# Kernel tuning notes

Measured on AMD Instinct MI355X. Metric: run time of the kernel, lower is better.

## Reference

```python
import jax, jax.numpy as jnp
import numpy as np

B, T, N, D = 1, 128, 32768, 1024


def setup_inputs() -> dict:
    key = jax.random.key(0)
    k1, k2 = jax.random.split(key)
    inputs = jax.random.normal(k1, (B, N, D), dtype=jnp.float32)
    # Nested tag->token coverage: tag i covers tokens [i*s, N). This guarantees
    # each tag keeps s exclusive tokens after the 'direct string' deduction,
    # so the row-normalization never divides by zero (matches real DOM data).
    s = N // T
    tok = jnp.arange(N)
    ttt = (tok[None, :] >= (jnp.arange(T) * s)[:, None]).astype(jnp.float32)  # (T, N)
    tag_to_token = jnp.broadcast_to(ttt[None], (B, T, N)).astype(jnp.float32)
    # Tag adjacency: self-loops + sparse random children.
    rand = jax.random.bernoulli(k2, 0.05, (T, T))
    gat_mask = (jnp.eye(T, dtype=bool) | rand).astype(jnp.int32)[None]  # (B, T, T)
    return {"inputs": inputs, "tag_to_token": tag_to_token, "gat_mask": gat_mask}


def deduce_direct_string(tag_to_token):
    # temp[i] = binary[i] - sum_{j>i} binary[j]  (original loop reads unmodified suffix rows)
    binary = (tag_to_token > 0).astype(tag_to_token.dtype)
    suffix_incl = jnp.flip(jnp.cumsum(jnp.flip(binary, axis=1), axis=1), axis=1)
    temp = binary - (suffix_incl - binary)
    temp = jnp.where(temp > 0, temp, 0.0)
    return temp / jnp.sum(temp, axis=2, keepdims=True)


def deduce_child(gat_mask):
    # Faithful to the torch nested loop (valid for B == 1).
    L = gat_mask.shape[1]

    def outer(i, child):
        child = child.at[:, i].set(gat_mask[:, i])

        def inner(j, c):
            temp = c[:, j][:, None, :] * gat_mask[:, j][:, None, :]  # (B,1,L)
            return ((c - temp) > 0).astype(c.dtype)

        return jax.lax.fori_loop(i + 1, L, inner, child)

    return jax.lax.fori_loop(0, L, outer, jnp.zeros_like(gat_mask))


def reference(inputs, tag_to_token, gat_mask):
    gm = gat_mask.astype(inputs.dtype)
    t2t = deduce_direct_string(tag_to_token)          # (B, T, N)
    child = deduce_child(gm)                          # (B, T, T)
    outputs = jnp.matmul(t2t, inputs)                 # (B, T, D)
    Tn = outputs.shape[1]

    # Triangular recurrence, i = T-1 ... 0; row i reads already-updated rows > i.
    def step(o, i):
        row = jnp.einsum('bt,btd->bd', child[:, i], o)
        return o.at[:, i].set(row), None

    outputs, _ = jax.lax.scan(step, outputs, jnp.arange(Tn - 1, -1, -1))
    return outputs
```

## Files before the change

### kernel.cpp

```cpp
#include <hip/hip_runtime.h>

#define NTOK 32768
#define NTAG 128
#define DDIM 1024
#define TPB 32


__global__ __launch_bounds__(256) void k_zero(const int* __restrict__ gm,
                                              float* __restrict__ P,
                                              int* __restrict__ cnt,
                                              unsigned* __restrict__ maskT) {
    const int tid = threadIdx.x;
    const int gid = blockIdx.x * 256 + tid;
    reinterpret_cast<float4*>(P)[gid] = make_float4(0.f, 0.f, 0.f, 0.f);
    if (gid < NTAG) cnt[gid] = 0;

    if (blockIdx.x == 1 || blockIdx.x == 2) {
        const int idx = (blockIdx.x - 1) * 256 + tid;
        const int l = idx & 15;
        const int iw = (idx >> 4) & 3;
        const int k = idx >> 6;
        const int colg = 16 * k + l;
        unsigned w = 0;
#pragma unroll
        for (int ib = 0; ib < 32; ++ib)
            w |= (unsigned)(gm[(iw * 32 + ib) * NTAG + colg] != 0) << ib;
        maskT[idx] = w;
    }
}

__global__ __launch_bounds__(256) void k_fused(const float* __restrict__ inp,
                                               const float* __restrict__ t2t,
                                               float* __restrict__ P,
                                               int* __restrict__ cnt) {
    __shared__ int part[8][TPB];
    __shared__ int tags[TPB];
    const int tid = threadIdx.x;
    const int n0 = blockIdx.x * TPB;

    {
        const int c = tid >> 5;
        const int n = tid & 31;
        int m = -1;
#pragma unroll
        for (int j = 0; j < 16; ++j) {
            const int r = c * 16 + j;
            if (t2t[(size_t)r * NTOK + n0 + n] > 0.f) m = r;
        }
        part[c][n] = m;
    }
    __syncthreads();
    if (tid < TPB) {
        int m = -1;
#pragma unroll
        for (int cc = 0; cc < 8; ++cc) m = max(m, part[cc][tid]);
        tags[tid] = m;
    }
    __syncthreads();

    const int col = tid * 4;
    const float4* src = reinterpret_cast<const float4*>(inp) + (size_t)n0 * 256 + tid;

    float4 acc = make_float4(0.f, 0.f, 0.f, 0.f);
    int cur = tags[0];
    int runlen = 0;

#pragma unroll
    for (int half = 0; half < 2; ++half) {
        float4 v[16];
#pragma unroll
        for (int k = 0; k < 16; ++k)
            v[k] = src[(size_t)(half * 16 + k) * 256];
#pragma unroll
        for (int k = 0; k < 16; ++k) {
            const int tg = tags[half * 16 + k];
            if (tg != cur) {
                if (cur >= 0) {
                    float* p = P + (size_t)cur * DDIM + col;
                    atomicAdd(p + 0, acc.x);
                    atomicAdd(p + 1, acc.y);
                    atomicAdd(p + 2, acc.z);
                    atomicAdd(p + 3, acc.w);
                    if (tid == 0) atomicAdd(&cnt[cur], runlen);
                }
                acc = make_float4(0.f, 0.f, 0.f, 0.f);
                cur = tg;
                runlen = 0;
            }
            if (tg >= 0) {
                acc.x += v[k].x;
                acc.y += v[k].y;
                acc.z += v[k].z;
                acc.w += v[k].w;
                ++runlen;
            }
        }
    }
    if (cur >= 0) {
        float* p = P + (size_t)cur * DDIM + col;
        atomicAdd(p + 0, acc.x);
        atomicAdd(p + 1, acc.y);
        atomicAdd(p + 2, acc.z);
        atomicAdd(p + 3, acc.w);
        if (tid == 0) atomicAdd(&cnt[cur], runlen);
    }
}

template <int CTRL>
__device__ __forceinline__ float dpp_add(float x) {
    const int y = __builtin_amdgcn_update_dpp(0, __float_as_int(x), CTRL, 0xF, 0xF, true);
    return x + __int_as_float(y);
}

__global__ __launch_bounds__(64, 1) void k_recur(const float* __restrict__ P,
                                                 const unsigned* __restrict__ maskT,
                                                 const int* __restrict__ cnt,
                                                 float* __restrict__ out) {
    __shared__ float xpose[NTAG][5];
    const int L = threadIdx.x;
    const int g = L >> 4;
    const int l = L & 15;
    const int c0 = blockIdx.x * 4;

    unsigned mw[8][4];
#pragma unroll
    for (int k = 0; k < 8; ++k)
#pragma unroll
        for (int iw = 0; iw < 4; ++iw) mw[k][iw] = maskT[(k * 4 + iw) * 16 + l];

    const float ia = 1.0f / (float)cnt[L];
    const float ib_ = 1.0f / (float)cnt[64 + L];
    float4 pa = *reinterpret_cast<const float4*>(P + (size_t)L * DDIM + c0);
    float4 pb = *reinterpret_cast<const float4*>(P + (size_t)(64 + L) * DDIM + c0);
    xpose[L][0] = pa.x * ia;
    xpose[L][1] = pa.y * ia;
    xpose[L][2] = pa.z * ia;
    xpose[L][3] = pa.w * ia;
    xpose[64 + L][0] = pb.x * ib_;
    xpose[64 + L][1] = pb.y * ib_;
    xpose[64 + L][2] = pb.z * ib_;
    xpose[64 + L][3] = pb.w * ib_;
    __syncthreads();

    float o0 = xpose[l][g], o1 = xpose[16 + l][g];
    float o2 = xpose[32 + l][g], o3 = xpose[48 + l][g];
    float o4 = xpose[64 + l][g], o5 = xpose[80 + l][g];
    float o6 = xpose[96 + l][g], o7 = xpose[112 + l][g];

#define SECTION(IW, KU, IBHI, IBLO)                                         \
    _Pragma("unroll 2") for (int ib = IBHI; ib >= IBLO; --ib) {             \
        float sa = (float)((mw[0][IW] >> ib) & 1u) * o0;                    \
        sa += (float)((mw[1][IW] >> ib) & 1u) * o1;                         \
        sa += (float)((mw[2][IW] >> ib) & 1u) * o2;                         \
        sa += (float)((mw[3][IW] >> ib) & 1u) * o3;                         \
        float sb = (float)((mw[4][IW] >> ib) & 1u) * o4;                    \
        sb += (float)((mw[5][IW] >> ib) & 1u) * o5;                         \
        sb += (float)((mw[6][IW] >> ib) & 1u) * o6;                         \
        sb += (float)((mw[7][IW] >> ib) & 1u) * o7;                         \
        float s = sa + sb;                                                  \
        s = dpp_add<0xB1>(s);                           \
        s = dpp_add<0x4E>(s);                           \
        s = dpp_add<0x141>(s);                         \
        s = dpp_add<0x140>(s);  \
        if (l == (ib & 15)) o##KU = s;                                      \
    }

    SECTION(3, 7, 31, 16)
    SECTION(3, 6, 15, 0)
    SECTION(2, 5, 31, 16)
    SECTION(2, 4, 15, 0)
    SECTION(1, 3, 31, 16)
    SECTION(1, 2, 15, 0)
    SECTION(0, 1, 31, 16)
    SECTION(0, 0, 15, 0)
#undef SECTION

    __syncthreads();
    xpose[l][g] = o0;
    xpose[16 + l][g] = o1;
    xpose[32 + l][g] = o2;
    xpose[48 + l][g] = o3;
    xpose[64 + l][g] = o4;
    xpose[80 + l][g] = o5;
    xpose[96 + l][g] = o6;
    xpose[112 + l][g] = o7;
    __syncthreads();
    float4 ra, rb;
    ra.x = xpose[L][0];
    ra.y = xpose[L][1];
    ra.z = xpose[L][2];
    ra.w = xpose[L][3];
    rb.x = xpose[64 + L][0];
    rb.y = xpose[64 + L][1];
    rb.z = xpose[64 + L][2];
    rb.w = xpose[64 + L][3];
    *reinterpret_cast<float4*>(out + (size_t)L * DDIM + c0) = ra;
    *reinterpret_cast<float4*>(out + (size_t)(64 + L) * DDIM + c0) = rb;
}

extern "C" void kernel_launch(void* const* d_in, const int* in_sizes, int n_in,
                              void* d_out, int out_size, void* d_ws, size_t ws_size,
                              hipStream_t stream) {
    const float* inp = (const float*)d_in[0];
    const float* t2t = (const float*)d_in[1];
    const int* gm = (const int*)d_in[2];
    float* out = (float*)d_out;

    char* ws = (char*)d_ws;
    float* P = (float*)ws;
    int* cnt = (int*)(ws + 524288);
    unsigned* maskT = (unsigned*)(ws + 524800);

    k_zero<<<128, 256, 0, stream>>>(gm, P, cnt, maskT);
    k_fused<<<NTOK / TPB, 256, 0, stream>>>(inp, t2t, P, cnt);
    k_recur<<<DDIM / 4, 64, 0, stream>>>(P, maskT, cnt, out);
}
```

Measured before the change: 51.22 us.

## Precompute blocked triangular resolvent to batch recurrence in groups of eight rows

A setup kernel now solves each 8x8 diagonal block of the mask recurrence ahead of time and stores float coefficient rows RT, one row per tag. With those coefficients, the recurrence kernel can compute eight rows together from the group's pre-update values instead of running 128 strictly serial dependent steps. This shortens the critical dependency chain and lets the eight DPP reductions per group overlap. In exchange, each group reads float4 coefficient rows from global memory instead of bitmasks held in registers, and the zeroing launch shrinks from 128 blocks to 16.

```diff
diff --git a/kernel.cpp b/kernel.cpp
--- a/kernel.cpp
+++ b/kernel.cpp
@@ -6,27 +6,41 @@
 #define TPB 32
 
 
-__global__ __launch_bounds__(256) void k_zero(const int* __restrict__ gm,
-                                              float* __restrict__ P,
-                                              int* __restrict__ cnt,
-                                              unsigned* __restrict__ maskT) {
-    const int tid = threadIdx.x;
-    const int gid = blockIdx.x * 256 + tid;
-    reinterpret_cast<float4*>(P)[gid] = make_float4(0.f, 0.f, 0.f, 0.f);
-    if (gid < NTAG) cnt[gid] = 0;
-
-    if (blockIdx.x == 1 || blockIdx.x == 2) {
-        const int idx = (blockIdx.x - 1) * 256 + tid;
-        const int l = idx & 15;
-        const int iw = (idx >> 4) & 3;
-        const int k = idx >> 6;
-        const int colg = 16 * k + l;
-        unsigned w = 0;
-#pragma unroll
-        for (int ib = 0; ib < 32; ++ib)
-            w |= (unsigned)(gm[(iw * 32 + ib) * NTAG + colg] != 0) << ib;
-        maskT[idx] = w;
-    }
+__global__ __launch_bounds__(128) void k_rt(const int* __restrict__ gm,
+                                            float* __restrict__ P,
+                                            int* __restrict__ cnt,
+                                            float* __restrict__ RT) {
+    __shared__ float rt[8][NTAG];
+    __shared__ float gblk[8][8];
+    const int t = threadIdx.x;
+    const int b = blockIdx.x;
+    const int g0 = b * 8;
+
+    float4* P4 = reinterpret_cast<float4*>(P) + b * 2048 + t;
+#pragma unroll
+    for (int q = 0; q < 16; ++q) P4[q * 128] = make_float4(0.f, 0.f, 0.f, 0.f);
+    if (b == 0) cnt[t] = 0;
+
+    if (t < 64) gblk[t >> 3][t & 7] =
+        (float)(gm[(g0 + (t >> 3)) * NTAG + g0 + (t & 7)] != 0);
+    float grows[8];
+#pragma unroll
+    for (int jj = 0; jj < 8; ++jj)
+        grows[jj] = (float)(gm[(g0 + jj) * NTAG + t] != 0);
+    __syncthreads();
+
+#pragma unroll
+    for (int jj = 7; jj >= 0; --jj) {
+        const int j = g0 + jj;
+        float acc = (t > j && t < g0 + 8) ? 0.f : grows[jj];
+        for (int k = jj + 1; k < 8; ++k) acc += gblk[jj][k] * rt[k][t];
+        rt[jj][t] = acc;
+        __syncthreads();
+    }
+
+#pragma unroll
+    for (int jj = 0; jj < 8; ++jj)
+        RT[(g0 + jj) * NTAG + (t & 15) * 8 + (t >> 4)] = rt[jj][t];
 }
 
 __global__ __launch_bounds__(256) void k_fused(const float* __restrict__ inp,
@@ -113,7 +127,7 @@
 }
 
 __global__ __launch_bounds__(64, 1) void k_recur(const float* __restrict__ P,
-                                                 const unsigned* __restrict__ maskT,
+                                                 const float* __restrict__ RT,
                                                  const int* __restrict__ cnt,
                                                  float* __restrict__ out) {
     __shared__ float xpose[NTAG][5];
@@ -121,12 +135,6 @@
     const int g = L >> 4;
     const int l = L & 15;
     const int c0 = blockIdx.x * 4;
-
-    unsigned mw[8][4];
-#pragma unroll
-    for (int k = 0; k < 8; ++k)
-#pragma unroll
-        for (int iw = 0; iw < 4; ++iw) mw[k][iw] = maskT[(k * 4 + iw) * 16 + l];
 
     const float ia = 1.0f / (float)cnt[L];
     const float ib_ = 1.0f / (float)cnt[64 + L];
@@ -147,33 +155,42 @@
     float o4 = xpose[64 + l][g], o5 = xpose[80 + l][g];
     float o6 = xpose[96 + l][g], o7 = xpose[112 + l][g];
 
-#define SECTION(IW, KU, IBHI, IBLO)                                         \
-    _Pragma("unroll 2") for (int ib = IBHI; ib >= IBLO; --ib) {             \
-        float sa = (float)((mw[0][IW] >> ib) & 1u) * o0;                    \
-        sa += (float)((mw[1][IW] >> ib) & 1u) * o1;                         \
-        sa += (float)((mw[2][IW] >> ib) & 1u) * o2;                         \
-        sa += (float)((mw[3][IW] >> ib) & 1u) * o3;                         \
-        float sb = (float)((mw[4][IW] >> ib) & 1u) * o4;                    \
-        sb += (float)((mw[5][IW] >> ib) & 1u) * o5;                         \
-        sb += (float)((mw[6][IW] >> ib) & 1u) * o6;                         \
-        sb += (float)((mw[7][IW] >> ib) & 1u) * o7;                         \
-        float s = sa + sb;                                                  \
-        s = dpp_add<0xB1>(s);                           \
-        s = dpp_add<0x4E>(s);                           \
-        s = dpp_add<0x141>(s);                         \
-        s = dpp_add<0x140>(s);  \
-        if (l == (ib & 15)) o##KU = s;                                      \
-    }
-
-    SECTION(3, 7, 31, 16)
-    SECTION(3, 6, 15, 0)
-    SECTION(2, 5, 31, 16)
-    SECTION(2, 4, 15, 0)
-    SECTION(1, 3, 31, 16)
-    SECTION(1, 2, 15, 0)
-    SECTION(0, 1, 31, 16)
-    SECTION(0, 0, 15, 0)
-#undef SECTION
+#define GROUP_SECTION(KU)                                                      \
+    for (int it = 1; it >= 0; --it) {                                          \
+        const int jbase = KU * 16 + it * 8;                                    \
+        const int lbase = it * 8;                                              \
+        float4 ra[8], rb[8];                                                   \
+        _Pragma("unroll") for (int jj = 0; jj < 8; ++jj) {                     \
+            const float* rp = RT + (jbase + jj) * NTAG + l * 8;                \
+            ra[jj] = *reinterpret_cast<const float4*>(rp);                     \
+            rb[jj] = *reinterpret_cast<const float4*>(rp + 4);                 \
+        }                                                                      \
+        float s[8];                                                            \
+        _Pragma("unroll") for (int jj = 0; jj < 8; ++jj) {                     \
+            float sa = ra[jj].x * o0 + ra[jj].y * o1 + ra[jj].z * o2 +         \
+                       ra[jj].w * o3;                                          \
+            float sb = rb[jj].x * o4 + rb[jj].y * o5 + rb[jj].z * o6 +         \
+                       rb[jj].w * o7;                                          \
+            float ss = sa + sb;                                                \
+            ss = dpp_add<0xB1>(ss);                        \
+            ss = dpp_add<0x4E>(ss);                        \
+            ss = dpp_add<0x141>(ss);                      \
+            ss = dpp_add<0x140>(ss);            \
+            s[jj] = ss;                                                        \
+        }                                                                      \
+        _Pragma("unroll") for (int jj = 0; jj < 8; ++jj)                       \
+            if (l == lbase + jj) o##KU = s[jj];                                \
+    }
+
+    GROUP_SECTION(7)
+    GROUP_SECTION(6)
+    GROUP_SECTION(5)
+    GROUP_SECTION(4)
+    GROUP_SECTION(3)
+    GROUP_SECTION(2)
+    GROUP_SECTION(1)
+    GROUP_SECTION(0)
+#undef GROUP_SECTION
 
     __syncthreads();
     xpose[l][g] = o0;
@@ -209,9 +226,9 @@
     char* ws = (char*)d_ws;
     float* P = (float*)ws;
     int* cnt = (int*)(ws + 524288);
-    unsigned* maskT = (unsigned*)(ws + 524800);
-
-    k_zero<<<128, 256, 0, stream>>>(gm, P, cnt, maskT);
+    float* RT = (float*)(ws + 524800);
+
+    k_rt<<<16, 128, 0, stream>>>(gm, P, cnt, RT);
     k_fused<<<NTOK / TPB, 256, 0, stream>>>(inp, t2t, P, cnt);
-    k_recur<<<DDIM / 4, 64, 0, stream>>>(P, maskT, cnt, out);
-}
+    k_recur<<<DDIM / 4, 64, 0, stream>>>(P, RT, cnt, out);
+}
```

Measured after the change: 51.03 us. Within noise of the previous version (-0.4%).
